# Performance work log

Measured on AMD Instinct MI355X. Metric: run time of the kernel, lower is better.

Reference implementation:

```python
import jax, jax.numpy as jnp
import numpy as np

D, D_SEQ, D_HEAD, N_HEAD = 256, 1280, 48, 8
N_NODE, B_GRAPH, S_LEN = 2048, 8, 1024
HDH = N_HEAD * D_HEAD  # 384
SCALE = float(np.sqrt(D_HEAD))
LN_EPS = 1e-5


def setup_inputs() -> dict:
    key = jax.random.key(0)
    ks = jax.random.split(key, 12)
    node = jax.random.normal(ks[0], (N_NODE, D), dtype=jnp.float32)
    emb = jax.random.normal(ks[1], (B_GRAPH, S_LEN, D_SEQ), dtype=jnp.float32)
    mask = jax.random.randint(ks[2], (B_GRAPH, S_LEN), 0, 2, dtype=jnp.int32)
    batch = jnp.sort(jax.random.randint(ks[3], (N_NODE,), 0, B_GRAPH, dtype=jnp.int64))
    def lin(k, fan_in, fan_out):
        lim = 1.0 / np.sqrt(fan_in)
        return jax.random.uniform(k, (fan_in, fan_out), jnp.float32, -lim, lim)
    return {
        "node": node,
        "packed_sequence_emb": emb,
        "packed_sequence_mask": mask,
        "batch": batch,
        "ln_g": jnp.ones((D,), jnp.float32),
        "ln_b": jnp.zeros((D,), jnp.float32),
        "Wq": lin(ks[4], D, HDH),
        "Wk": lin(ks[5], D_SEQ, HDH),
        "Wv": lin(ks[6], D_SEQ, HDH),
        "Wg": lin(ks[7], D, HDH),
        "bg": jnp.zeros((HDH,), jnp.float32),
        "Wback": lin(ks[8], HDH, D),
        "bback": jnp.zeros((D,), jnp.float32),
    }


def _layernorm(x, g, b):
    mu = jnp.mean(x, axis=-1, keepdims=True)
    var = jnp.mean(jnp.square(x - mu), axis=-1, keepdims=True)
    return (x - mu) * jax.lax.rsqrt(var + LN_EPS) * g + b


def reference(node, packed_sequence_emb, packed_sequence_mask, batch,
              ln_g, ln_b, Wq, Wk, Wv, Wg, bg, Wback, bback):
    N = node.shape[0]
    y = _layernorm(node, ln_g, ln_b)                                   # [N, D]
    q = (y @ Wq).reshape(N, N_HEAD, D_HEAD)                            # [N, H, Dh]
    k = (packed_sequence_emb @ Wk).reshape(B_GRAPH, S_LEN, N_HEAD, D_HEAD)
    v = (packed_sequence_emb @ Wv).reshape(B_GRAPH, S_LEN, N_HEAD, D_HEAD)

    # scores[n, s, h] = <q[n,h], k[batch[n], s, h]> / sqrt(Dh)
    scores_all = jnp.einsum('nhd,bshd->nbsh', q, k) / SCALE            # [N, B, S, H]
    scores = jnp.take_along_axis(
        scores_all, batch[:, None, None, None].astype(jnp.int32), axis=1
    )[:, 0]                                                            # [N, S, H]

    # masked softmax over sequence axis (dim=1), mask broadcast over heads
    mask_f = packed_sequence_mask[batch].astype(scores.dtype)[:, :, None]  # [N, S, 1]
    s_max = jnp.max(jnp.where(mask_f > 0, scores, -jnp.inf), axis=1, keepdims=True)
    e = jnp.exp(scores - s_max) * mask_f
    w = e / (jnp.sum(e, axis=1, keepdims=True) + 1e-9)                 # [N, S, H]

    # out[n,h,d] = sum_s w[n,s,h] * v[batch[n], s, h, d]
    feat_all = jnp.einsum('nsh,bshd->nbhd', w, v)                      # [N, B, H, Dh]
    feat = jnp.take_along_axis(
        feat_all, batch[:, None, None, None].astype(jnp.int32), axis=1
    )[:, 0]                                                            # [N, H, Dh]

    gate = jax.nn.sigmoid(y @ Wg + bg).reshape(N, N_HEAD, D_HEAD)
    new = (gate * feat).reshape(N, HDH) @ Wback + bback
    return node + new
```

## Files before the change

kernel.cpp:

```cpp
#include <hip/hip_runtime.h>
#include <hip/hip_bf16.h>
#include <math.h>

#define D 256
#define D_SEQ 1280
#define D_HEAD 48
#define N_HEAD 8
#define HDH 384
#define N_NODE 2048
#define B_GRAPH 8
#define S_LEN 1024
#define LN_EPS 1e-5f
#define QSCALE (0.14433756729740643f * 1.4426950408889634f)
#define KVN 768
#define QGN 768
#define QROWS (N_NODE + 16)
#define TPG 40
#define NWL (TPG * 8)
#define PAD_T 164864

typedef unsigned short u16;
typedef __attribute__((ext_vector_type(8))) short short8;
typedef __attribute__((ext_vector_type(4))) short short4v;
typedef __attribute__((ext_vector_type(4))) unsigned short ushort4v;
typedef __attribute__((ext_vector_type(4))) float floatx4;

__device__ __forceinline__ u16 f2bf(float f) {
    unsigned int x = __float_as_uint(f);
    x += 0x7fff + ((x >> 16) & 1);
    return (u16)(x >> 16);
}

__device__ __forceinline__ void load_lds16(const u16* g, u16* lds) {
    __builtin_amdgcn_global_load_lds(
        (const __attribute__((address_space(1))) unsigned int*)g,
        (__attribute__((address_space(3))) unsigned int*)lds, 16, 0, 0);
}

__global__ __launch_bounds__(256)
void prep(const float* __restrict__ emb, u16* __restrict__ embb,
          const float* __restrict__ node, const float* __restrict__ ln_g,
          const float* __restrict__ ln_b, u16* __restrict__ yb,
          const float* __restrict__ Wk, const float* __restrict__ Wv,
          const float* __restrict__ Wq, const float* __restrict__ Wg,
          const float* __restrict__ Wback,
          u16* __restrict__ WT, u16* __restrict__ WT2, u16* __restrict__ WbT,
          const int* __restrict__ batch, const int* __restrict__ mask,
          int* __restrict__ ranges, int* __restrict__ wl,
          int* __restrict__ kvwl, int* __restrict__ scnt,
          u16* __restrict__ Kp, u16* __restrict__ Qb) {
    const int bx = blockIdx.x;
    const int tid = threadIdx.x;
    if (bx < 512) {
        const int b = bx >> 6, chunk = bx & 63;
        __shared__ unsigned long long words[16];
        __shared__ int wpre[17];
        #pragma unroll
        for (int c = 0; c < 4; ++c) {
            const int s = c * 256 + tid;
            const unsigned long long bal = __ballot(mask[b * S_LEN + s] != 0);
            if ((tid & 63) == 0) words[c * 4 + (tid >> 6)] = bal;
        }
        __syncthreads();
        if (tid == 0) {
            int a = 0;
            #pragma unroll
            for (int w = 0; w < 16; ++w) { wpre[w] = a; a += __popcll(words[w]); }
            wpre[16] = a;
        }
        __syncthreads();
        const int cnt = wpre[16];
        const int ce = (cnt + 127) & ~127;
        const int r = chunk * 16 + (tid >> 4);
        const int sub = tid & 15;
        const unsigned long long w = words[r >> 6];
        const bool on = (w >> (r & 63)) & 1ull;
        if (on) {
            const int rank = wpre[r >> 6] +
                __popcll(w & ((1ull << (r & 63)) - 1ull));
            const float* src = &emb[((size_t)b * S_LEN + r) * D_SEQ];
            u16* dst = &embb[((size_t)b * S_LEN + rank) * D_SEQ];
            #pragma unroll
            for (int it = 0; it < 10; ++it) {
                const int off = it * 128 + sub * 8;
                const float4 a = *(const float4*)&src[off];
                const float4 b4 = *(const float4*)&src[off + 4];
                union { u16 u[8]; int4 v; } p;
                p.u[0]=f2bf(a.x); p.u[1]=f2bf(a.y); p.u[2]=f2bf(a.z); p.u[3]=f2bf(a.w);
                p.u[4]=f2bf(b4.x); p.u[5]=f2bf(b4.y); p.u[6]=f2bf(b4.z); p.u[7]=f2bf(b4.w);
                *(int4*)&dst[off] = p.v;
            }
        }
        const int c2 = chunk * 16 + (tid >> 4);
        if (c2 >= cnt && c2 < ce) {
            u16* dst = &embb[((size_t)b * S_LEN + c2) * D_SEQ];
            const int4 z = {0, 0, 0, 0};
            #pragma unroll
            for (int it = 0; it < 10; ++it)
                *(int4*)&dst[it * 128 + sub * 8] = z;
        }
        return;
    }
    if (bx < 2560) {
        const int n = bx - 512, t = tid;
        float x = node[n * D + t];
        float s = x, sq = x * x;
        #pragma unroll
        for (int o = 32; o > 0; o >>= 1) {
            s  += __shfl_down(s, o);
            sq += __shfl_down(sq, o);
        }
        __shared__ float ss[4], sqs[4];
        if ((t & 63) == 0) { ss[t >> 6] = s; sqs[t >> 6] = sq; }
        __syncthreads();
        float S  = ss[0] + ss[1] + ss[2] + ss[3];
        float SQ = sqs[0] + sqs[1] + sqs[2] + sqs[3];
        float mu  = S * (1.f / D);
        float var = SQ * (1.f / D) - mu * mu;
        float inv = rsqrtf(var + LN_EPS);
        yb[n * D + t] = f2bf((x - mu) * inv * ln_g[t] + ln_b[t]);
        return;
    }
    if (bx < 3808) {
        int u = bx - 2560;
        const float* W; u16* WTo; int K, kx, ny, Ncols;
        if (u < 480)      { W = Wk;    WTo = WT;                       K = D_SEQ; Ncols = HDH; kx = u % 40; ny = u / 40; }
        else if (u < 960) { u -= 480;  W = Wv; WTo = WT + (size_t)HDH * D_SEQ; K = D_SEQ; Ncols = HDH; kx = u % 40; ny = u / 40; }
        else if (u < 1056){ u -= 960;  W = Wq; WTo = WT2;              K = D;   Ncols = HDH; kx = u % 8;  ny = u / 8; }
        else if (u < 1152){ u -= 1056; W = Wg; WTo = WT2 + (size_t)HDH * D; K = D; Ncols = HDH; kx = u % 8; ny = u / 8; }
        else              { u -= 1152; W = Wback; WTo = WbT;           K = HDH; Ncols = D;   kx = u % 12; ny = u / 12; }
        const int k0 = kx * 32, n0 = ny * 32;
        __shared__ float tile[32][33];
        const int tx = tid & 31, ty = tid >> 5;
        #pragma unroll
        for (int i = 0; i < 32; i += 8)
            tile[ty + i][tx] = W[(size_t)(k0 + ty + i) * Ncols + n0 + tx];
        __syncthreads();
        #pragma unroll
        for (int i = 0; i < 32; i += 8)
            WTo[(size_t)(n0 + ty + i) * K + k0 + tx] = f2bf(tile[tx][ty + i]);
        return;
    }
    if (bx == 3808) {
        const int t = tid;
        __shared__ int msum[8][32];
        __shared__ int mcnt[8];
        const int g = t >> 5, ii = t & 31;
        int p = 0;
        #pragma unroll
        for (int k = 0; k < 32; ++k) p += mask[g * S_LEN + k * 32 + ii];
        msum[g][ii] = p;
        if (t <= B_GRAPH) {
            int lo = 0, hi = N_NODE;
            while (lo < hi) {
                int mid = (lo + hi) >> 1;
                if (batch[mid] < t) lo = mid + 1; else hi = mid;
            }
            ranges[t] = lo;
        }
        __syncthreads();
        if (t < 8) {
            int s = 0;
            #pragma unroll
            for (int k = 0; k < 32; ++k) s += msum[t][k];
            mcnt[t] = s;
            scnt[t] = s;
        }
        __syncthreads();
        if (t < B_GRAPH) {
            const int s = ranges[t];
            const int ntile = (ranges[t + 1] - s + 15) >> 4;
            for (int i = 0; i < TPG; ++i)
                wl[i * 8 + t] = (i < ntile) ? ((t << 16) | (s + i * 16)) : -1;
            const int tc = (mcnt[t] + 127) >> 7;
            for (int i = 0; i < 8; ++i)
                kvwl[i * 8 + t] = (i < tc) ? (t * S_LEN + i * 128) : -1;
        }
        return;
    }
    const int t = (bx - 3809) * 256 + tid;
    const int4 z = {0, 0, 0, 0};
    if (t < 131072) {
        const int row = t >> 1, half = t & 1;
        *(int4*)&Kp[(size_t)row * 64 + 48 + half * 8] = z;
    } else if (t < 164096) {
        const int u = t - 131072;
        const int row = u >> 1, half = u & 1;
        *(int4*)&Qb[(size_t)row * 64 + 48 + half * 8] = z;
    } else {
        const int u = t - 164096;
        const int row = u / 6, c = u - row * 6;
        const int hh = row >> 4, m = 2048 + (row & 15);
        *(int4*)&Qb[((size_t)hh * QROWS + m) * 64 + c * 8] = z;
    }
}

__global__ __launch_bounds__(256)
void kvqg_gemm(const u16* __restrict__ A, const u16* __restrict__ WT,
               u16* __restrict__ Kp, u16* __restrict__ V4,
               const u16* __restrict__ Ab, const u16* __restrict__ WT2,
               const float* __restrict__ bg, u16* __restrict__ Qb,
               float* __restrict__ gate, const int* __restrict__ kvwl) {
    __shared__ __align__(16) u16 As[128 * 32];
    __shared__ __align__(16) u16 Bs[128 * 32];
    const int tid = threadIdx.x;
    const int lane = tid & 63, wave = tid >> 6;
    const int wm64 = (wave >> 1) * 64, wn64 = (wave & 1) * 64;
    const int lm = lane & 15, lq = lane >> 4;

    if (blockIdx.x < 384) {
        const int e = kvwl[blockIdx.x / 6];
        if (e < 0) return;
        const int m0 = e;
        const int n0 = (blockIdx.x % 6) * 128;

        floatx4 acc[4][4] = {};

        const int srow = lane >> 2, scol = (lane & 3) * 8;
        const u16* ag  = &A[(size_t)(m0 + wave * 16 + srow) * D_SEQ + scol];
        const u16* ag2 = ag + (size_t)64 * D_SEQ;
        const u16* bgp = &WT[(size_t)(n0 + wave * 16 + srow) * D_SEQ + scol];
        const u16* bg2 = bgp + (size_t)64 * D_SEQ;
        u16* asb  = &As[wave * 512];
        u16* asb2 = &As[2048 + wave * 512];
        u16* bsb  = &Bs[wave * 512];
        u16* bsb2 = &Bs[2048 + wave * 512];

        for (int k0 = 0; k0 < D_SEQ; k0 += 32) {
            __syncthreads();
            load_lds16(ag + k0, asb);
            load_lds16(ag2 + k0, asb2);
            load_lds16(bgp + k0, bsb);
            load_lds16(bg2 + k0, bsb2);
            __syncthreads();

            short8 af[4], bfr[4];
            #pragma unroll
            for (int i = 0; i < 4; ++i)
                af[i] = *(const short8*)&As[(wm64 + i * 16 + lm) * 32 + lq * 8];
            #pragma unroll
            for (int j = 0; j < 4; ++j)
                bfr[j] = *(const short8*)&Bs[(wn64 + j * 16 + lm) * 32 + lq * 8];
            #pragma unroll
            for (int i = 0; i < 4; ++i)
                #pragma unroll
                for (int j = 0; j < 4; ++j)
                    acc[i][j] = __builtin_amdgcn_mfma_f32_16x16x32_bf16(
                        af[i], bfr[j], acc[i][j], 0, 0, 0);
        }

        #pragma unroll
        for (int i = 0; i < 4; ++i) {
            const int mrow = m0 + wm64 + i * 16 + lq * 4;
            const int bb = mrow >> 10, s = mrow & 1023;
            #pragma unroll
            for (int j = 0; j < 4; ++j) {
                const int n = n0 + wn64 + j * 16 + lm;
                if (n < HDH) {
                    const int hh = n / 48, dd = n - hh * 48;
                    u16* kp = &Kp[(((size_t)(bb * N_HEAD + hh)) * S_LEN + s) * 64 + dd];
                    kp[0]   = f2bf(acc[i][j][0]);
                    kp[64]  = f2bf(acc[i][j][1]);
                    kp[128] = f2bf(acc[i][j][2]);
                    kp[192] = f2bf(acc[i][j][3]);
                } else {
                    const int nv = n - HDH;
                    const int hh = nv / 48, dd = nv - hh * 48;
                    ushort4v pk;
                    pk[0] = f2bf(acc[i][j][0]); pk[1] = f2bf(acc[i][j][1]);
                    pk[2] = f2bf(acc[i][j][2]); pk[3] = f2bf(acc[i][j][3]);
                    *(ushort4v*)&V4[(((size_t)(bb * N_HEAD + hh)) * (S_LEN / 4) + (s >> 2)) * 192 + dd * 4] = pk;
                }
            }
        }
        return;
    }

    {
        const int u = blockIdx.x - 384;
        const int m0 = (u / 6) * 128, n0 = (u % 6) * 128;

        floatx4 acc[4][4] = {};
        const int sr = tid >> 2;
        const int sc = (tid & 3) * 8;

        for (int k0 = 0; k0 < D; k0 += 32) {
            const int4 a0 = *(const int4*)&Ab[(size_t)(m0 + sr) * D + k0 + sc];
            const int4 a1 = *(const int4*)&Ab[(size_t)(m0 + sr + 64) * D + k0 + sc];
            const int4 b0 = *(const int4*)&WT2[(size_t)(n0 + sr) * D + k0 + sc];
            const int4 b1 = *(const int4*)&WT2[(size_t)(n0 + sr + 64) * D + k0 + sc];
            __syncthreads();
            *(int4*)&As[sr * 32 + sc] = a0;
            *(int4*)&As[(sr + 64) * 32 + sc] = a1;
            *(int4*)&Bs[sr * 32 + sc] = b0;
            *(int4*)&Bs[(sr + 64) * 32 + sc] = b1;
            __syncthreads();

            short8 af[4], bfr[4];
            #pragma unroll
            for (int i = 0; i < 4; ++i)
                af[i] = *(const short8*)&As[(wm64 + i * 16 + lm) * 32 + lq * 8];
            #pragma unroll
            for (int i = 0; i < 4; ++i)
                bfr[i] = *(const short8*)&Bs[(wn64 + i * 16 + lm) * 32 + lq * 8];
            #pragma unroll
            for (int i = 0; i < 4; ++i)
                #pragma unroll
                for (int j = 0; j < 4; ++j)
                    acc[i][j] = __builtin_amdgcn_mfma_f32_16x16x32_bf16(
                        af[i], bfr[j], acc[i][j], 0, 0, 0);
        }

        #pragma unroll
        for (int i = 0; i < 4; ++i) {
            const int mb = m0 + wm64 + i * 16 + lq * 4;
            #pragma unroll
            for (int j = 0; j < 4; ++j) {
                const int n = n0 + wn64 + j * 16 + lm;
                #pragma unroll
                for (int r = 0; r < 4; ++r) {
                    const int m = mb + r;
                    const float v = acc[i][j][r];
                    if (n < HDH) {
                        const int hh = n / 48, dd = n - hh * 48;
                        Qb[((size_t)hh * QROWS + m) * 64 + dd] = f2bf(v * QSCALE);
                    } else {
                        const int ng = n - HDH;
                        gate[(size_t)m * HDH + ng] = 1.f / (1.f + __expf(-(v + bg[ng])));
                    }
                }
            }
        }
    }
}

__global__ __launch_bounds__(256)
void back_gemm(const u16* __restrict__ Ab, const u16* __restrict__ Bt,
               const float* __restrict__ bias, const float* __restrict__ resid,
               float* __restrict__ C) {
    __shared__ __align__(16) u16 As[128 * 32];
    __shared__ __align__(16) u16 Bs[128 * 32];
    const int tid = threadIdx.x;
    const int lane = tid & 63, wave = tid >> 6;
    const int wm = (wave >> 1) * 64, wn = (wave & 1) * 64;
    const int m0 = blockIdx.y * 128, n0 = blockIdx.x * 128;
    const int lm = lane & 15, lq = lane >> 4;

    floatx4 acc[4][4] = {};
    const int sr = tid >> 2;
    const int sc = (tid & 3) * 8;

    for (int k0 = 0; k0 < HDH; k0 += 32) {
        const int4 a0 = *(const int4*)&Ab[(size_t)(m0 + sr) * HDH + k0 + sc];
        const int4 a1 = *(const int4*)&Ab[(size_t)(m0 + sr + 64) * HDH + k0 + sc];
        const int4 b0 = *(const int4*)&Bt[(size_t)(n0 + sr) * HDH + k0 + sc];
        const int4 b1 = *(const int4*)&Bt[(size_t)(n0 + sr + 64) * HDH + k0 + sc];
        __syncthreads();
        *(int4*)&As[sr * 32 + sc] = a0;
        *(int4*)&As[(sr + 64) * 32 + sc] = a1;
        *(int4*)&Bs[sr * 32 + sc] = b0;
        *(int4*)&Bs[(sr + 64) * 32 + sc] = b1;
        __syncthreads();

        short8 af[4], bfr[4];
        #pragma unroll
        for (int i = 0; i < 4; ++i)
            af[i] = *(const short8*)&As[(wm + i * 16 + lm) * 32 + lq * 8];
        #pragma unroll
        for (int i = 0; i < 4; ++i)
            bfr[i] = *(const short8*)&Bs[(wn + i * 16 + lm) * 32 + lq * 8];
        #pragma unroll
        for (int i = 0; i < 4; ++i)
            #pragma unroll
            for (int j = 0; j < 4; ++j)
                acc[i][j] = __builtin_amdgcn_mfma_f32_16x16x32_bf16(
                    af[i], bfr[j], acc[i][j], 0, 0, 0);
    }

    #pragma unroll
    for (int i = 0; i < 4; ++i) {
        const int mb = m0 + wm + i * 16 + lq * 4;
        #pragma unroll
        for (int j = 0; j < 4; ++j) {
            const int n = n0 + wn + j * 16 + lm;
            #pragma unroll
            for (int r = 0; r < 4; ++r) {
                const int m = mb + r;
                C[(size_t)m * D + n] = acc[i][j][r] + bias[n] + resid[(size_t)m * D + n];
            }
        }
    }
}

struct Pref {
    short8 k0, k1;
    short4v v0, v1, v2;
};

__device__ __forceinline__ Pref ldpref(const u16* kbase, const u16* vbase,
                                       int s, int lm, int lq) {
    Pref p;
    const u16* kr = &kbase[(size_t)(s + lm) * 64];
    p.k0 = *(const short8*)&kr[lq * 8];
    p.k1 = *(const short8*)&kr[32 + lq * 8];
    const size_t vo = (size_t)((s >> 2) + lq) * 192;
    p.v0 = *(const short4v*)&vbase[vo];
    p.v1 = *(const short4v*)&vbase[vo + 64];
    p.v2 = *(const short4v*)&vbase[vo + 128];
    return p;
}

__global__ __launch_bounds__(256)
void attn_mfma(const u16* __restrict__ Qb, const u16* __restrict__ Kp,
               const u16* __restrict__ V4, const int* __restrict__ scnt,
               const int* __restrict__ ranges, const int* __restrict__ wl,
               float* __restrict__ Pacc, float* __restrict__ Pl) {
    const int e = wl[blockIdx.x];
    if (e < 0) return;
    const int b = e >> 16, n0 = e & 0xffff;
    const int h = blockIdx.y, sp = blockIdx.z;
    const int nend = ranges[b + 1];
    const int NT = min(16, nend - n0);

    const int tid = threadIdx.x;
    const int wave = tid >> 6, lane = tid & 63;
    const int lm = lane & 15, lq = lane >> 4;
    const int bh = b * N_HEAD + h;

    const u16* qrow = &Qb[((size_t)h * QROWS + n0 + lm) * 64];
    const short8 qf0 = *(const short8*)&qrow[lq * 8];
    const short8 qf1 = *(const short8*)&qrow[32 + lq * 8];

    const u16* kbase = &Kp[(size_t)bh * S_LEN * 64];
    const u16* vbase = &V4[(size_t)bh * (S_LEN / 4) * 192 + (size_t)lm * 4];

    const int cnt = scnt[b];
    const int T = (cnt + 15) >> 4;
    const int j = sp * 4 + wave;
    const int nt = (j < T) ? (((T - 1 - j) >> 3) + 1) : 0;

    float l_i = 0.f;
    floatx4 acc0 = {}, acc1 = {}, acc2 = {};

    Pref pA, pB;
    if (nt > 0) pA = ldpref(kbase, vbase, j * 16, lm, lq);
    if (nt > 1) pB = ldpref(kbase, vbase, (j + 8) * 16, lm, lq);

    int t = 0;
    auto step = [&](Pref& P) {
        const int s0 = (j + t * 8) * 16;
        floatx4 st = {};
        st = __builtin_amdgcn_mfma_f32_16x16x32_bf16(P.k0, qf0, st, 0, 0, 0);
        st = __builtin_amdgcn_mfma_f32_16x16x32_bf16(P.k1, qf1, st, 0, 0, 0);
        const short4v v0 = P.v0, v1 = P.v1, v2 = P.v2;
        if (t + 2 < nt) P = ldpref(kbase, vbase, (j + (t + 2) * 8) * 16, lm, lq);

        const int rem = cnt - s0 - lq * 4;
        const float p0 = rem > 0 ? exp2f(st[0]) : 0.f;
        const float p1 = rem > 1 ? exp2f(st[1]) : 0.f;
        const float p2 = rem > 2 ? exp2f(st[2]) : 0.f;
        const float p3 = rem > 3 ? exp2f(st[3]) : 0.f;
        l_i += (p0 + p1) + (p2 + p3);

        union { __hip_bfloat162 h2[2]; short4v v; } pu;
        pu.h2[0] = __float22bfloat162_rn(make_float2(p0, p1));
        pu.h2[1] = __float22bfloat162_rn(make_float2(p2, p3));

        acc0 = __builtin_amdgcn_mfma_f32_16x16x16bf16_1k(v0, pu.v, acc0, 0, 0, 0);
        acc1 = __builtin_amdgcn_mfma_f32_16x16x16bf16_1k(v1, pu.v, acc1, 0, 0, 0);
        acc2 = __builtin_amdgcn_mfma_f32_16x16x16bf16_1k(v2, pu.v, acc2, 0, 0, 0);
        ++t;
    };
    while (t < nt) {
        step(pA);
        if (t < nt) step(pB);
    }

    l_i += __shfl_xor(l_i, 16);
    l_i += __shfl_xor(l_i, 32);

    __shared__ float sl[4][64];
    __shared__ float sacc[4][3][4][64];
    sl[wave][lane] = l_i;
    #pragma unroll
    for (int r = 0; r < 4; ++r) {
        sacc[wave][0][r][lane] = acc0[r];
        sacc[wave][1][r][lane] = acc1[r];
        sacc[wave][2][r][lane] = acc2[r];
    }
    __syncthreads();
    if (wave < 3 && lm < NT) {
        const int dt = wave;
        const float L = sl[0][lane] + sl[1][lane] + sl[2][lane] + sl[3][lane];
        const size_t o = (size_t)(n0 + lm) * HDH + h * 48 + dt * 16 + lq * 4;
        float4 ov;
        ov.x = sacc[0][dt][0][lane] + sacc[1][dt][0][lane] +
               sacc[2][dt][0][lane] + sacc[3][dt][0][lane];
        ov.y = sacc[0][dt][1][lane] + sacc[1][dt][1][lane] +
               sacc[2][dt][1][lane] + sacc[3][dt][1][lane];
        ov.z = sacc[0][dt][2][lane] + sacc[1][dt][2][lane] +
               sacc[2][dt][2][lane] + sacc[3][dt][2][lane];
        ov.w = sacc[0][dt][3][lane] + sacc[1][dt][3][lane] +
               sacc[2][dt][3][lane] + sacc[3][dt][3][lane];
        *(float4*)&Pacc[(size_t)sp * N_NODE * HDH + o] = ov;
        if (wave == 0 && lq == 0)
            Pl[(size_t)sp * N_NODE * N_HEAD + (n0 + lm) * N_HEAD + h] = L;
    }
}

__global__ __launch_bounds__(256)
void fuse_kernel(const float* __restrict__ Pacc, const float* __restrict__ Pl,
                 const float* __restrict__ gate, u16* __restrict__ gfeatb) {
    const size_t i4 = ((size_t)blockIdx.x * 256 + threadIdx.x) * 4;
    const int nh = (int)(i4 / 48);
    const float4 a = *(const float4*)&Pacc[i4];
    const float4 c = *(const float4*)&Pacc[(size_t)N_NODE * HDH + i4];
    const float4 g = *(const float4*)&gate[i4];
    const float L = Pl[nh] + Pl[N_NODE * N_HEAD + nh];
    const float inv = 1.f / (L + 1e-9f);
    union { __hip_bfloat162 h2[2]; ushort4v v; } r2;
    r2.h2[0] = __float22bfloat162_rn(make_float2((a.x + c.x) * inv * g.x,
                                                 (a.y + c.y) * inv * g.y));
    r2.h2[1] = __float22bfloat162_rn(make_float2((a.z + c.z) * inv * g.z,
                                                 (a.w + c.w) * inv * g.w));
    *(ushort4v*)&gfeatb[i4] = r2.v;
}

extern "C" void kernel_launch(void* const* d_in, const int* in_sizes, int n_in,
                              void* d_out, int out_size, void* d_ws, size_t ws_size,
                              hipStream_t stream) {
    const float* node  = (const float*)d_in[0];
    const float* emb   = (const float*)d_in[1];
    const int*   mask  = (const int*)d_in[2];
    const int*   batch = (const int*)d_in[3];
    const float* ln_g  = (const float*)d_in[4];
    const float* ln_b  = (const float*)d_in[5];
    const float* Wq    = (const float*)d_in[6];
    const float* Wk    = (const float*)d_in[7];
    const float* Wv    = (const float*)d_in[8];
    const float* Wg    = (const float*)d_in[9];
    const float* bg    = (const float*)d_in[10];
    const float* Wback = (const float*)d_in[11];
    const float* bback = (const float*)d_in[12];
    float* out = (float*)d_out;

    float* ws    = (float*)d_ws;
    float* gate  = ws;
    float* Pacc  = gate + (size_t)N_NODE * HDH;
    float* Pl    = Pacc + (size_t)2 * N_NODE * HDH;
    u16*   gfeatb = (u16*)(Pl + (size_t)2 * N_NODE * N_HEAD);
    u16*   yb    = gfeatb + (size_t)N_NODE * HDH;
    u16*   WT    = yb + (size_t)N_NODE * D;
    u16*   WT2   = WT + (size_t)KVN * D_SEQ;
    u16*   WbT   = WT2 + (size_t)QGN * D;
    u16*   Qb    = WbT + (size_t)D * HDH;
    u16*   Kp    = Qb + (size_t)N_HEAD * QROWS * 64;
    u16*   V4    = Kp + (size_t)B_GRAPH * N_HEAD * S_LEN * 64;
    u16*   embb  = V4 + (size_t)B_GRAPH * N_HEAD * (S_LEN / 4) * 192;
    int*   ranges = (int*)(embb + (size_t)B_GRAPH * S_LEN * D_SEQ);
    int*   wl    = ranges + 16;
    int*   kvwl  = wl + NWL;
    int*   scnt  = kvwl + 64;

    prep<<<3809 + PAD_T / 256, 256, 0, stream>>>(
        emb, embb, node, ln_g, ln_b, yb, Wk, Wv, Wq, Wg, Wback,
        WT, WT2, WbT, batch, mask, ranges, wl, kvwl, scnt, Kp, Qb);
    kvqg_gemm<<<480, 256, 0, stream>>>(embb, WT, Kp, V4, yb, WT2, bg, Qb, gate, kvwl);
    attn_mfma<<<dim3(NWL, N_HEAD, 2), 256, 0, stream>>>(
        Qb, Kp, V4, scnt, ranges, wl, Pacc, Pl);
    fuse_kernel<<<(N_NODE * HDH) / (256 * 4), 256, 0, stream>>>(
        Pacc, Pl, gate, gfeatb);
    back_gemm<<<dim3(D / 128, N_NODE / 128), 256, 0, stream>>>(
        gfeatb, WbT, bback, node, out);
}
```

Measured before the change: 176.1 us.

## Fuse split-softmax combine into back GEMM; widen K-tile to 64 with swizzled LDS

The separate fuse_kernel is removed. back_gemm now reads the two partial attention accumulators, normaliser and gate directly, combines them, converts to bf16 and writes the A tile into LDS, which avoids one launch and a bf16 intermediate round trip. All three GEMM paths also move from a 32-wide to a 64-wide K tile with XOR-swizzled LDS layouts and direct global-to-LDS loads, halving the barrier count and reducing bank conflicts. The cost is doubled LDS use per block. back_gemm also now does combine work that is redundant across its two N-tile blocks.

```diff
diff --git a/kernel.cpp b/kernel.cpp
--- a/kernel.cpp
+++ b/kernel.cpp
@@ -201,12 +201,16 @@
                const u16* __restrict__ Ab, const u16* __restrict__ WT2,
                const float* __restrict__ bg, u16* __restrict__ Qb,
                float* __restrict__ gate, const int* __restrict__ kvwl) {
-    __shared__ __align__(16) u16 As[128 * 32];
-    __shared__ __align__(16) u16 Bs[128 * 32];
+    __shared__ __align__(16) u16 As[128 * 64];
+    __shared__ __align__(16) u16 Bs[128 * 64];
     const int tid = threadIdx.x;
     const int lane = tid & 63, wave = tid >> 6;
     const int wm64 = (wave >> 1) * 64, wn64 = (wave & 1) * 64;
     const int lm = lane & 15, lq = lane >> 4;
+    const int r8 = lane >> 3;
+    const int csw = ((lane & 7) ^ (r8 & 7)) * 8;
+    const int s0 = (lq ^ (lm & 7)) * 8;
+    const int s1 = s0 ^ (4 * 8);
 
     if (blockIdx.x < 384) {
         const int e = kvwl[blockIdx.x / 6];
@@ -216,37 +220,39 @@
 
         floatx4 acc[4][4] = {};
 
-        const int srow = lane >> 2, scol = (lane & 3) * 8;
-        const u16* ag  = &A[(size_t)(m0 + wave * 16 + srow) * D_SEQ + scol];
-        const u16* ag2 = ag + (size_t)64 * D_SEQ;
-        const u16* bgp = &WT[(size_t)(n0 + wave * 16 + srow) * D_SEQ + scol];
-        const u16* bg2 = bgp + (size_t)64 * D_SEQ;
-        u16* asb  = &As[wave * 512];
-        u16* asb2 = &As[2048 + wave * 512];
-        u16* bsb  = &Bs[wave * 512];
-        u16* bsb2 = &Bs[2048 + wave * 512];
-
-        for (int k0 = 0; k0 < D_SEQ; k0 += 32) {
+        const u16* ag  = &A[(size_t)(m0 + wave * 32 + r8) * D_SEQ + csw];
+        const u16* bgp = &WT[(size_t)(n0 + wave * 32 + r8) * D_SEQ + csw];
+
+        for (int k0 = 0; k0 < D_SEQ; k0 += 64) {
             __syncthreads();
-            load_lds16(ag + k0, asb);
-            load_lds16(ag2 + k0, asb2);
-            load_lds16(bgp + k0, bsb);
-            load_lds16(bg2 + k0, bsb2);
+            #pragma unroll
+            for (int it = 0; it < 4; ++it) {
+                load_lds16(ag  + (size_t)(it * 8) * D_SEQ + k0, &As[(wave * 32 + it * 8) * 64]);
+                load_lds16(bgp + (size_t)(it * 8) * D_SEQ + k0, &Bs[(wave * 32 + it * 8) * 64]);
+            }
             __syncthreads();
 
-            short8 af[4], bfr[4];
-            #pragma unroll
-            for (int i = 0; i < 4; ++i)
-                af[i] = *(const short8*)&As[(wm64 + i * 16 + lm) * 32 + lq * 8];
-            #pragma unroll
-            for (int j = 0; j < 4; ++j)
-                bfr[j] = *(const short8*)&Bs[(wn64 + j * 16 + lm) * 32 + lq * 8];
-            #pragma unroll
-            for (int i = 0; i < 4; ++i)
+            short8 af[4][2], bfv[4][2];
+            #pragma unroll
+            for (int i = 0; i < 4; ++i) {
+                const int R = wm64 + i * 16 + lm;
+                af[i][0] = *(const short8*)&As[R * 64 + s0];
+                af[i][1] = *(const short8*)&As[R * 64 + s1];
+            }
+            #pragma unroll
+            for (int j = 0; j < 4; ++j) {
+                const int R = wn64 + j * 16 + lm;
+                bfv[j][0] = *(const short8*)&Bs[R * 64 + s0];
+                bfv[j][1] = *(const short8*)&Bs[R * 64 + s1];
+            }
+            #pragma unroll
+            for (int h = 0; h < 2; ++h)
                 #pragma unroll
-                for (int j = 0; j < 4; ++j)
-                    acc[i][j] = __builtin_amdgcn_mfma_f32_16x16x32_bf16(
-                        af[i], bfr[j], acc[i][j], 0, 0, 0);
+                for (int i = 0; i < 4; ++i)
+                    #pragma unroll
+                    for (int j = 0; j < 4; ++j)
+                        acc[i][j] = __builtin_amdgcn_mfma_f32_16x16x32_bf16(
+                            af[i][h], bfv[j][h], acc[i][j], 0, 0, 0);
         }
 
         #pragma unroll
@@ -281,34 +287,40 @@
         const int m0 = (u / 6) * 128, n0 = (u % 6) * 128;
 
         floatx4 acc[4][4] = {};
-        const int sr = tid >> 2;
-        const int sc = (tid & 3) * 8;
-
-        for (int k0 = 0; k0 < D; k0 += 32) {
-            const int4 a0 = *(const int4*)&Ab[(size_t)(m0 + sr) * D + k0 + sc];
-            const int4 a1 = *(const int4*)&Ab[(size_t)(m0 + sr + 64) * D + k0 + sc];
-            const int4 b0 = *(const int4*)&WT2[(size_t)(n0 + sr) * D + k0 + sc];
-            const int4 b1 = *(const int4*)&WT2[(size_t)(n0 + sr + 64) * D + k0 + sc];
+
+        const u16* ag  = &Ab[(size_t)(m0 + wave * 32 + r8) * D + csw];
+        const u16* bgp = &WT2[(size_t)(n0 + wave * 32 + r8) * D + csw];
+
+        for (int k0 = 0; k0 < D; k0 += 64) {
             __syncthreads();
-            *(int4*)&As[sr * 32 + sc] = a0;
-            *(int4*)&As[(sr + 64) * 32 + sc] = a1;
-            *(int4*)&Bs[sr * 32 + sc] = b0;
-            *(int4*)&Bs[(sr + 64) * 32 + sc] = b1;
+            #pragma unroll
+            for (int it = 0; it < 4; ++it) {
+                load_lds16(ag  + (size_t)(it * 8) * D + k0, &As[(wave * 32 + it * 8) * 64]);
+                load_lds16(bgp + (size_t)(it * 8) * D + k0, &Bs[(wave * 32 + it * 8) * 64]);
+            }
             __syncthreads();
 
-            short8 af[4], bfr[4];
-            #pragma unroll
-            for (int i = 0; i < 4; ++i)
-                af[i] = *(const short8*)&As[(wm64 + i * 16 + lm) * 32 + lq * 8];
-            #pragma unroll
-            for (int i = 0; i < 4; ++i)
-                bfr[i] = *(const short8*)&Bs[(wn64 + i * 16 + lm) * 32 + lq * 8];
-            #pragma unroll
-            for (int i = 0; i < 4; ++i)
+            short8 af[4][2], bfv[4][2];
+            #pragma unroll
+            for (int i = 0; i < 4; ++i) {
+                const int R = wm64 + i * 16 + lm;
+                af[i][0] = *(const short8*)&As[R * 64 + s0];
+                af[i][1] = *(const short8*)&As[R * 64 + s1];
+            }
+            #pragma unroll
+            for (int j = 0; j < 4; ++j) {
+                const int R = wn64 + j * 16 + lm;
+                bfv[j][0] = *(const short8*)&Bs[R * 64 + s0];
+                bfv[j][1] = *(const short8*)&Bs[R * 64 + s1];
+            }
+            #pragma unroll
+            for (int h = 0; h < 2; ++h)
                 #pragma unroll
-                for (int j = 0; j < 4; ++j)
-                    acc[i][j] = __builtin_amdgcn_mfma_f32_16x16x32_bf16(
-                        af[i], bfr[j], acc[i][j], 0, 0, 0);
+                for (int i = 0; i < 4; ++i)
+                    #pragma unroll
+                    for (int j = 0; j < 4; ++j)
+                        acc[i][j] = __builtin_amdgcn_mfma_f32_16x16x32_bf16(
+                            af[i][h], bfv[j][h], acc[i][j], 0, 0, 0);
         }
 
         #pragma unroll
@@ -335,46 +347,84 @@
 }
 
 __global__ __launch_bounds__(256)
-void back_gemm(const u16* __restrict__ Ab, const u16* __restrict__ Bt,
+void back_gemm(const float* __restrict__ Pacc, const float* __restrict__ Pl,
+               const float* __restrict__ gate, const u16* __restrict__ Bt,
                const float* __restrict__ bias, const float* __restrict__ resid,
                float* __restrict__ C) {
-    __shared__ __align__(16) u16 As[128 * 32];
-    __shared__ __align__(16) u16 Bs[128 * 32];
+    __shared__ __align__(16) u16 As[128 * 64];
+    __shared__ __align__(16) u16 Bs[128 * 64];
     const int tid = threadIdx.x;
     const int lane = tid & 63, wave = tid >> 6;
     const int wm = (wave >> 1) * 64, wn = (wave & 1) * 64;
     const int m0 = blockIdx.y * 128, n0 = blockIdx.x * 128;
     const int lm = lane & 15, lq = lane >> 4;
+    const int r8 = lane >> 3;
+    const int csw = ((lane & 7) ^ (r8 & 7)) * 8;
+    const int s0 = (lq ^ (lm & 7)) * 8;
+    const int s1 = s0 ^ (4 * 8);
+
+    const int arow = tid >> 3;
+    const int asl  = tid & 7;
+    const int asw  = (asl ^ (arow & 7)) * 8;
+
+    const u16* bt0 = &Bt[(size_t)(n0 + wave * 32 + r8) * HDH + csw];
 
     floatx4 acc[4][4] = {};
-    const int sr = tid >> 2;
-    const int sc = (tid & 3) * 8;
-
-    for (int k0 = 0; k0 < HDH; k0 += 32) {
-        const int4 a0 = *(const int4*)&Ab[(size_t)(m0 + sr) * HDH + k0 + sc];
-        const int4 a1 = *(const int4*)&Ab[(size_t)(m0 + sr + 64) * HDH + k0 + sc];
-        const int4 b0 = *(const int4*)&Bt[(size_t)(n0 + sr) * HDH + k0 + sc];
-        const int4 b1 = *(const int4*)&Bt[(size_t)(n0 + sr + 64) * HDH + k0 + sc];
-        __syncthreads();
-        *(int4*)&As[sr * 32 + sc] = a0;
-        *(int4*)&As[(sr + 64) * 32 + sc] = a1;
-        *(int4*)&Bs[sr * 32 + sc] = b0;
-        *(int4*)&Bs[(sr + 64) * 32 + sc] = b1;
-        __syncthreads();
-
-        short8 af[4], bfr[4];
-        #pragma unroll
-        for (int i = 0; i < 4; ++i)
-            af[i] = *(const short8*)&As[(wm + i * 16 + lm) * 32 + lq * 8];
-        #pragma unroll
-        for (int i = 0; i < 4; ++i)
-            bfr[i] = *(const short8*)&Bs[(wn + i * 16 + lm) * 32 + lq * 8];
-        #pragma unroll
-        for (int i = 0; i < 4; ++i)
-            #pragma unroll
-            for (int j = 0; j < 4; ++j)
-                acc[i][j] = __builtin_amdgcn_mfma_f32_16x16x32_bf16(
-                    af[i], bfr[j], acc[i][j], 0, 0, 0);
+
+    for (int k0 = 0; k0 < HDH; k0 += 64) {
+        __syncthreads();
+        #pragma unroll
+        for (int it = 0; it < 4; ++it)
+            load_lds16(bt0 + (size_t)(it * 8) * HDH + k0, &Bs[(wave * 32 + it * 8) * 64]);
+        const int col = k0 + asl * 8;
+        const int hh = col / 48;
+        #pragma unroll
+        for (int s = 0; s < 4; ++s) {
+            const int row = arow + 32 * s;
+            const int m = m0 + row;
+            const float L = Pl[m * N_HEAD + hh] + Pl[N_NODE * N_HEAD + m * N_HEAD + hh];
+            const float inv = 1.f / (L + 1e-9f);
+            const size_t o = (size_t)m * HDH + col;
+            const float4 pa0 = *(const float4*)&Pacc[o];
+            const float4 pa1 = *(const float4*)&Pacc[o + 4];
+            const float4 pb0 = *(const float4*)&Pacc[(size_t)N_NODE * HDH + o];
+            const float4 pb1 = *(const float4*)&Pacc[(size_t)N_NODE * HDH + o + 4];
+            const float4 g0 = *(const float4*)&gate[o];
+            const float4 g1 = *(const float4*)&gate[o + 4];
+            union { u16 u[8]; int4 v; } p;
+            p.u[0] = f2bf((pa0.x + pb0.x) * inv * g0.x);
+            p.u[1] = f2bf((pa0.y + pb0.y) * inv * g0.y);
+            p.u[2] = f2bf((pa0.z + pb0.z) * inv * g0.z);
+            p.u[3] = f2bf((pa0.w + pb0.w) * inv * g0.w);
+            p.u[4] = f2bf((pa1.x + pb1.x) * inv * g1.x);
+            p.u[5] = f2bf((pa1.y + pb1.y) * inv * g1.y);
+            p.u[6] = f2bf((pa1.z + pb1.z) * inv * g1.z);
+            p.u[7] = f2bf((pa1.w + pb1.w) * inv * g1.w);
+            *(int4*)&As[row * 64 + asw] = p.v;
+        }
+        __syncthreads();
+
+        short8 af[4][2], bfv[4][2];
+        #pragma unroll
+        for (int i = 0; i < 4; ++i) {
+            const int R = wm + i * 16 + lm;
+            af[i][0] = *(const short8*)&As[R * 64 + s0];
+            af[i][1] = *(const short8*)&As[R * 64 + s1];
+        }
+        #pragma unroll
+        for (int j = 0; j < 4; ++j) {
+            const int R = wn + j * 16 + lm;
+            bfv[j][0] = *(const short8*)&Bs[R * 64 + s0];
+            bfv[j][1] = *(const short8*)&Bs[R * 64 + s1];
+        }
+        #pragma unroll
+        for (int h = 0; h < 2; ++h)
+            #pragma unroll
+            for (int i = 0; i < 4; ++i)
+                #pragma unroll
+                for (int j = 0; j < 4; ++j)
+                    acc[i][j] = __builtin_amdgcn_mfma_f32_16x16x32_bf16(
+                        af[i][h], bfv[j][h], acc[i][j], 0, 0, 0);
     }
 
     #pragma unroll
@@ -508,24 +558,6 @@
     }
 }
 
-__global__ __launch_bounds__(256)
-void fuse_kernel(const float* __restrict__ Pacc, const float* __restrict__ Pl,
-                 const float* __restrict__ gate, u16* __restrict__ gfeatb) {
-    const size_t i4 = ((size_t)blockIdx.x * 256 + threadIdx.x) * 4;
-    const int nh = (int)(i4 / 48);
-    const float4 a = *(const float4*)&Pacc[i4];
-    const float4 c = *(const float4*)&Pacc[(size_t)N_NODE * HDH + i4];
-    const float4 g = *(const float4*)&gate[i4];
-    const float L = Pl[nh] + Pl[N_NODE * N_HEAD + nh];
-    const float inv = 1.f / (L + 1e-9f);
-    union { __hip_bfloat162 h2[2]; ushort4v v; } r2;
-    r2.h2[0] = __float22bfloat162_rn(make_float2((a.x + c.x) * inv * g.x,
-                                                 (a.y + c.y) * inv * g.y));
-    r2.h2[1] = __float22bfloat162_rn(make_float2((a.z + c.z) * inv * g.z,
-                                                 (a.w + c.w) * inv * g.w));
-    *(ushort4v*)&gfeatb[i4] = r2.v;
-}
-
 extern "C" void kernel_launch(void* const* d_in, const int* in_sizes, int n_in,
                               void* d_out, int out_size, void* d_ws, size_t ws_size,
                               hipStream_t stream) {
@@ -568,8 +600,6 @@
     kvqg_gemm<<<480, 256, 0, stream>>>(embb, WT, Kp, V4, yb, WT2, bg, Qb, gate, kvwl);
     attn_mfma<<<dim3(NWL, N_HEAD, 2), 256, 0, stream>>>(
         Qb, Kp, V4, scnt, ranges, wl, Pacc, Pl);
-    fuse_kernel<<<(N_NODE * HDH) / (256 * 4), 256, 0, stream>>>(
-        Pacc, Pl, gate, gfeatb);
     back_gemm<<<dim3(D / 128, N_NODE / 128), 256, 0, stream>>>(
-        gfeatb, WbT, bback, node, out);
-}
+        Pacc, Pl, gate, WbT, bback, node, out);
+}
```

New measurement: 181.2 us. +2.9%, slower.

## Drop sequence split in attention and fuse normalize-gate epilogue into it

Applied to the files above, without the earlier changes.

The attention kernel no longer splits the sequence dimension across two blocks. Each block's four waves now stride over all sequence tiles, so the block already holds the full softmax denominator and weighted sum. The normalize, gate multiply and bf16 conversion move into the attention epilogue, which removes the separate fuse kernel and its float partial-sum round trip through memory. The cost is half as many attention blocks, so each block runs a longer serial loop and the GPU has less parallelism to hide latency.

```diff
diff --git a/kernel.cpp b/kernel.cpp
--- a/kernel.cpp
+++ b/kernel.cpp
@@ -414,11 +414,11 @@
 void attn_mfma(const u16* __restrict__ Qb, const u16* __restrict__ Kp,
                const u16* __restrict__ V4, const int* __restrict__ scnt,
                const int* __restrict__ ranges, const int* __restrict__ wl,
-               float* __restrict__ Pacc, float* __restrict__ Pl) {
+               const float* __restrict__ gate, u16* __restrict__ gfeatb) {
     const int e = wl[blockIdx.x];
     if (e < 0) return;
     const int b = e >> 16, n0 = e & 0xffff;
-    const int h = blockIdx.y, sp = blockIdx.z;
+    const int h = blockIdx.y;
     const int nend = ranges[b + 1];
     const int NT = min(16, nend - n0);
 
@@ -436,24 +436,24 @@
 
     const int cnt = scnt[b];
     const int T = (cnt + 15) >> 4;
-    const int j = sp * 4 + wave;
-    const int nt = (j < T) ? (((T - 1 - j) >> 3) + 1) : 0;
+    const int j = wave;
+    const int nt = (j < T) ? (((T - 1 - j) >> 2) + 1) : 0;
 
     float l_i = 0.f;
     floatx4 acc0 = {}, acc1 = {}, acc2 = {};
 
     Pref pA, pB;
     if (nt > 0) pA = ldpref(kbase, vbase, j * 16, lm, lq);
-    if (nt > 1) pB = ldpref(kbase, vbase, (j + 8) * 16, lm, lq);
+    if (nt > 1) pB = ldpref(kbase, vbase, (j + 4) * 16, lm, lq);
 
     int t = 0;
     auto step = [&](Pref& P) {
-        const int s0 = (j + t * 8) * 16;
+        const int s0 = (j + t * 4) * 16;
         floatx4 st = {};
         st = __builtin_amdgcn_mfma_f32_16x16x32_bf16(P.k0, qf0, st, 0, 0, 0);
         st = __builtin_amdgcn_mfma_f32_16x16x32_bf16(P.k1, qf1, st, 0, 0, 0);
         const short4v v0 = P.v0, v1 = P.v1, v2 = P.v2;
-        if (t + 2 < nt) P = ldpref(kbase, vbase, (j + (t + 2) * 8) * 16, lm, lq);
+        if (t + 2 < nt) P = ldpref(kbase, vbase, (j + (t + 2) * 4) * 16, lm, lq);
 
         const int rem = cnt - s0 - lq * 4;
         const float p0 = rem > 0 ? exp2f(st[0]) : 0.f;
@@ -492,7 +492,9 @@
     if (wave < 3 && lm < NT) {
         const int dt = wave;
         const float L = sl[0][lane] + sl[1][lane] + sl[2][lane] + sl[3][lane];
+        const float inv = 1.f / (L + 1e-9f);
         const size_t o = (size_t)(n0 + lm) * HDH + h * 48 + dt * 16 + lq * 4;
+        const float4 g = *(const float4*)&gate[o];
         float4 ov;
         ov.x = sacc[0][dt][0][lane] + sacc[1][dt][0][lane] +
                sacc[2][dt][0][lane] + sacc[3][dt][0][lane];
@@ -502,28 +504,13 @@
                sacc[2][dt][2][lane] + sacc[3][dt][2][lane];
         ov.w = sacc[0][dt][3][lane] + sacc[1][dt][3][lane] +
                sacc[2][dt][3][lane] + sacc[3][dt][3][lane];
-        *(float4*)&Pacc[(size_t)sp * N_NODE * HDH + o] = ov;
-        if (wave == 0 && lq == 0)
-            Pl[(size_t)sp * N_NODE * N_HEAD + (n0 + lm) * N_HEAD + h] = L;
-    }
-}
-
-__global__ __launch_bounds__(256)
-void fuse_kernel(const float* __restrict__ Pacc, const float* __restrict__ Pl,
-                 const float* __restrict__ gate, u16* __restrict__ gfeatb) {
-    const size_t i4 = ((size_t)blockIdx.x * 256 + threadIdx.x) * 4;
-    const int nh = (int)(i4 / 48);
-    const float4 a = *(const float4*)&Pacc[i4];
-    const float4 c = *(const float4*)&Pacc[(size_t)N_NODE * HDH + i4];
-    const float4 g = *(const float4*)&gate[i4];
-    const float L = Pl[nh] + Pl[N_NODE * N_HEAD + nh];
-    const float inv = 1.f / (L + 1e-9f);
-    union { __hip_bfloat162 h2[2]; ushort4v v; } r2;
-    r2.h2[0] = __float22bfloat162_rn(make_float2((a.x + c.x) * inv * g.x,
-                                                 (a.y + c.y) * inv * g.y));
-    r2.h2[1] = __float22bfloat162_rn(make_float2((a.z + c.z) * inv * g.z,
-                                                 (a.w + c.w) * inv * g.w));
-    *(ushort4v*)&gfeatb[i4] = r2.v;
+        union { __hip_bfloat162 h2[2]; ushort4v v; } r2;
+        r2.h2[0] = __float22bfloat162_rn(make_float2(ov.x * inv * g.x,
+                                                     ov.y * inv * g.y));
+        r2.h2[1] = __float22bfloat162_rn(make_float2(ov.z * inv * g.z,
+                                                     ov.w * inv * g.w));
+        *(ushort4v*)&gfeatb[o] = r2.v;
+    }
 }
 
 extern "C" void kernel_launch(void* const* d_in, const int* in_sizes, int n_in,
@@ -566,10 +553,8 @@
         emb, embb, node, ln_g, ln_b, yb, Wk, Wv, Wq, Wg, Wback,
         WT, WT2, WbT, batch, mask, ranges, wl, kvwl, scnt, Kp, Qb);
     kvqg_gemm<<<480, 256, 0, stream>>>(embb, WT, Kp, V4, yb, WT2, bg, Qb, gate, kvwl);
-    attn_mfma<<<dim3(NWL, N_HEAD, 2), 256, 0, stream>>>(
-        Qb, Kp, V4, scnt, ranges, wl, Pacc, Pl);
-    fuse_kernel<<<(N_NODE * HDH) / (256 * 4), 256, 0, stream>>>(
-        Pacc, Pl, gate, gfeatb);
+    attn_mfma<<<dim3(NWL, N_HEAD), 256, 0, stream>>>(
+        Qb, Kp, V4, scnt, ranges, wl, gate, gfeatb);
     back_gemm<<<dim3(D / 128, N_NODE / 128), 256, 0, stream>>>(
         gfeatb, WbT, bback, node, out);
 }
```

Measured after the change: 170.2 us. 1.03x faster.
